# Optimization experiments

Hardware: AMD Instinct MI355X
Metric: run time of the kernel (lower is better)

## Reference

```python
import jax, jax.numpy as jnp
import numpy as np

N_EMBED = 16384
CODE_DIM = 32

def l2norm(t, eps=1e-12):
    return t / jnp.clip(jnp.linalg.norm(t, axis=-1, keepdims=True), eps)

def setup_inputs() -> dict:
    key = jax.random.key(0)
    k1, k2 = jax.random.split(key)
    z = jax.random.normal(k1, (8, 1024, CODE_DIM), dtype=jnp.float32)
    codebook = l2norm(jax.random.normal(k2, (N_EMBED, CODE_DIM), dtype=jnp.float32))
    return {"z": z, "codebook": codebook}

def reference(z, codebook):
    # z: [B, S, D]; codebook: [N, D]
    zn = l2norm(z)
    zf = zn.reshape(-1, zn.shape[-1])  # [B*S, D]
    d = (jnp.sum(zf * zf, axis=1, keepdims=True)
         + jnp.sum(codebook * codebook, axis=1)
         - 2.0 * jnp.einsum('bd,nd->bn', zf, codebook))  # [B*S, N]
    encoding_indices = jnp.argmin(d, axis=1)  # [B*S]
    z_q = codebook[encoding_indices]  # [B*S, D]
    return z_q, encoding_indices
```

## Files before the change

### kernel.cpp

```cpp
#include <hip/hip_runtime.h>
#include <math.h>

#define M_ROWS   8192
#define N_CODES  16384
#define D_DIM    32
#define NTHREADS 256

#define DELTA_MARGIN  2e-4f

#define NCHUNK       16
#define CHUNK_CODES  (N_CODES / NCHUNK)
#define SCAN_SLOTS   256

typedef short bf16x8 __attribute__((ext_vector_type(8)));
typedef float f32x4  __attribute__((ext_vector_type(4)));

__device__ inline unsigned short bf16_rne(float f) {
    unsigned u = __float_as_uint(f);
    unsigned r = u + 0x7FFFu + ((u >> 16) & 1u);
    return (unsigned short)(r >> 16);
}

__device__ inline void pack_pair(float f0, float f1, unsigned& hi, unsigned& lo) {
    unsigned short h0 = bf16_rne(f0), h1 = bf16_rne(f1);
    float r0 = f0 - __uint_as_float((unsigned)h0 << 16);
    float r1 = f1 - __uint_as_float((unsigned)h1 << 16);
    unsigned short l0 = bf16_rne(r0), l1 = bf16_rne(r1);
    hi = (unsigned)h0 | ((unsigned)h1 << 16);
    lo = (unsigned)l0 | ((unsigned)l1 << 16);
}

__global__ void vq_prep_pack(const float* __restrict__ z,
                             const float* __restrict__ codebook,
                             float* __restrict__ zn, float* __restrict__ zz,
                             float* __restrict__ cc,
                             unsigned* __restrict__ chi, unsigned* __restrict__ clo,
                             unsigned* __restrict__ zhi, unsigned* __restrict__ zlo,
                             int* __restrict__ todo_cnt) {
    int gid = blockIdx.x * NTHREADS + threadIdx.x;
    if (gid == 0) *todo_cnt = 0;
    if (blockIdx.x < 64) {
        const float4* r4 = reinterpret_cast<const float4*>(codebook + (size_t)gid * D_DIM);
        float4 v[8];
#pragma unroll
        for (int h = 0; h < 8; ++h) v[h] = r4[h];
        float s = 0.f;
#pragma unroll
        for (int h = 0; h < 8; ++h) {
            s = fmaf(v[h].x, v[h].x, s);
            s = fmaf(v[h].y, v[h].y, s);
            s = fmaf(v[h].z, v[h].z, s);
            s = fmaf(v[h].w, v[h].w, s);
        }
        cc[gid] = s;
#pragma unroll
        for (int h = 0; h < 8; ++h) {
            unsigned hi0, lo0, hi1, lo1;
            pack_pair(v[h].x, v[h].y, hi0, lo0);
            pack_pair(v[h].z, v[h].w, hi1, lo1);
            chi[gid * 16 + 2 * h]     = hi0;  clo[gid * 16 + 2 * h]     = lo0;
            chi[gid * 16 + 2 * h + 1] = hi1;  clo[gid * 16 + 2 * h + 1] = lo1;
        }
    } else {
        int r = gid - N_CODES;
        const float4* r4 = reinterpret_cast<const float4*>(z + (size_t)r * D_DIM);
        float4 v[8];
#pragma unroll
        for (int h = 0; h < 8; ++h) v[h] = r4[h];
        float s = 0.f;
#pragma unroll
        for (int h = 0; h < 8; ++h) {
            s = fmaf(v[h].x, v[h].x, s);
            s = fmaf(v[h].y, v[h].y, s);
            s = fmaf(v[h].z, v[h].z, s);
            s = fmaf(v[h].w, v[h].w, s);
        }
        float norm = sqrtf(s);
        norm = fmaxf(norm, 1e-12f);
        float zs = 0.f;
        float4* zn4 = reinterpret_cast<float4*>(zn + (size_t)r * D_DIM);
#pragma unroll
        for (int h = 0; h < 8; ++h) {
            float4 w;
            w.x = v[h].x / norm;
            w.y = v[h].y / norm;
            w.z = v[h].z / norm;
            w.w = v[h].w / norm;
            zn4[h] = w;
            zs = fmaf(w.x, w.x, zs);
            zs = fmaf(w.y, w.y, zs);
            zs = fmaf(w.z, w.z, zs);
            zs = fmaf(w.w, w.w, zs);
            v[h] = w;
        }
        zz[r] = zs;
#pragma unroll
        for (int h = 0; h < 8; ++h) {
            unsigned hi0, lo0, hi1, lo1;
            pack_pair(v[h].x, v[h].y, hi0, lo0);
            pack_pair(v[h].z, v[h].w, hi1, lo1);
            zhi[r * 16 + 2 * h]     = hi0;  zlo[r * 16 + 2 * h]     = lo0;
            zhi[r * 16 + 2 * h + 1] = hi1;  zlo[r * 16 + 2 * h + 1] = lo1;
        }
    }
}

template <int NS>
__global__ __launch_bounds__(NTHREADS, 4)
void vq_mfma(const unsigned short* __restrict__ zhi,
             const unsigned short* __restrict__ zlo,
             const unsigned short* __restrict__ chi,
             const unsigned short* __restrict__ clo,
             float* __restrict__ pmax1, float* __restrict__ pmax2,
             int* __restrict__ pidx) {
    constexpr int SLICE_CODES = N_CODES / NS;
    constexpr int NPAIR = SLICE_CODES / 32;

    const int tid  = threadIdx.x;
    const int wave = tid >> 6;
    const int lane = tid & 63;
    const int rb    = blockIdx.x & 63;
    const int slice = blockIdx.x >> 6;

    const int row_w = rb * 128 + wave * 32;
    const int l15 = lane & 15;
    const int kg  = lane >> 4;
    const int kc  = kg * 8;

    const bf16x8 a_hi0 = *reinterpret_cast<const bf16x8*>(zhi + (size_t)(row_w + l15) * 32 + kc);
    const bf16x8 a_lo0 = *reinterpret_cast<const bf16x8*>(zlo + (size_t)(row_w + l15) * 32 + kc);
    const bf16x8 a_hi1 = *reinterpret_cast<const bf16x8*>(zhi + (size_t)(row_w + 16 + l15) * 32 + kc);
    const bf16x8 a_lo1 = *reinterpret_cast<const bf16x8*>(zlo + (size_t)(row_w + 16 + l15) * 32 + kc);

    const f32x4 zero4 = {0.f, 0.f, 0.f, 0.f};

    float max1[8], max2[8];
    int   idx1[8];
#pragma unroll
    for (int q = 0; q < 8; ++q) { max1[q] = -3.4e38f; max2[q] = -3.4e38f; idx1[q] = 0x7FFFFFFF; }

    auto argup = [&](const f32x4& accA, const f32x4& accB, int code) {
#pragma unroll
        for (int e = 0; e < 4; ++e) {
            float s0 = accA[e];
            max2[e] = __builtin_amdgcn_fmed3f(s0, max1[e], max2[e]);
            bool gt0 = s0 > max1[e];
            max1[e] = gt0 ? s0 : max1[e];
            idx1[e] = gt0 ? code : idx1[e];

            float s1 = accB[e];
            max2[4 + e] = __builtin_amdgcn_fmed3f(s1, max1[4 + e], max2[4 + e]);
            bool gt1 = s1 > max1[4 + e];
            max1[4 + e] = gt1 ? s1 : max1[4 + e];
            idx1[4 + e] = gt1 ? code : idx1[4 + e];
        }
    };
    auto pair_compute = [&](const bf16x8& b0h, const bf16x8& b0l,
                            const bf16x8& b1h, const bf16x8& b1l, int code) {
        f32x4 a00 = __builtin_amdgcn_mfma_f32_16x16x32_bf16(a_lo0, b0h, zero4, 0, 0, 0);
        f32x4 a01 = __builtin_amdgcn_mfma_f32_16x16x32_bf16(a_lo1, b0h, zero4, 0, 0, 0);
        f32x4 a10 = __builtin_amdgcn_mfma_f32_16x16x32_bf16(a_lo0, b1h, zero4, 0, 0, 0);
        f32x4 a11 = __builtin_amdgcn_mfma_f32_16x16x32_bf16(a_lo1, b1h, zero4, 0, 0, 0);
        a00 = __builtin_amdgcn_mfma_f32_16x16x32_bf16(a_hi0, b0l, a00, 0, 0, 0);
        a01 = __builtin_amdgcn_mfma_f32_16x16x32_bf16(a_hi1, b0l, a01, 0, 0, 0);
        a10 = __builtin_amdgcn_mfma_f32_16x16x32_bf16(a_hi0, b1l, a10, 0, 0, 0);
        a11 = __builtin_amdgcn_mfma_f32_16x16x32_bf16(a_hi1, b1l, a11, 0, 0, 0);
        a00 = __builtin_amdgcn_mfma_f32_16x16x32_bf16(a_hi0, b0h, a00, 0, 0, 0);
        a01 = __builtin_amdgcn_mfma_f32_16x16x32_bf16(a_hi1, b0h, a01, 0, 0, 0);
        a10 = __builtin_amdgcn_mfma_f32_16x16x32_bf16(a_hi0, b1h, a10, 0, 0, 0);
        a11 = __builtin_amdgcn_mfma_f32_16x16x32_bf16(a_hi1, b1h, a11, 0, 0, 0);
        argup(a00, a01, code);
        argup(a10, a11, code + 16);
    };

    int code = slice * SLICE_CODES + l15;
    bf16x8 b0h = *reinterpret_cast<const bf16x8*>(chi + (size_t)code * 32 + kc);
    bf16x8 b0l = *reinterpret_cast<const bf16x8*>(clo + (size_t)code * 32 + kc);
    bf16x8 b1h = *reinterpret_cast<const bf16x8*>(chi + (size_t)(code + 16) * 32 + kc);
    bf16x8 b1l = *reinterpret_cast<const bf16x8*>(clo + (size_t)(code + 16) * 32 + kc);

    for (int p = 0; p < NPAIR - 1; ++p) {
        const int ncode = code + 32;
        const bf16x8 nb0h = *reinterpret_cast<const bf16x8*>(chi + (size_t)ncode * 32 + kc);
        const bf16x8 nb0l = *reinterpret_cast<const bf16x8*>(clo + (size_t)ncode * 32 + kc);
        const bf16x8 nb1h = *reinterpret_cast<const bf16x8*>(chi + (size_t)(ncode + 16) * 32 + kc);
        const bf16x8 nb1l = *reinterpret_cast<const bf16x8*>(clo + (size_t)(ncode + 16) * 32 + kc);

        pair_compute(b0h, b0l, b1h, b1l, code);

        b0h = nb0h; b0l = nb0l; b1h = nb1h; b1l = nb1l; code = ncode;
    }
    pair_compute(b0h, b0l, b1h, b1l, code);

#pragma unroll
    for (int q = 0; q < 8; ++q) {
        float m1 = max1[q], m2 = max2[q];
        int   i1 = idx1[q];
#pragma unroll
        for (int off = 1; off < 16; off <<= 1) {
            float o1 = __shfl_xor(m1, off);
            float o2 = __shfl_xor(m2, off);
            int   oi = __shfl_xor(i1, off);
            float nm2 = fmaxf(fminf(m1, o1), fmaxf(m2, o2));
            if (o1 > m1 || (o1 == m1 && oi < i1)) { m1 = o1; i1 = oi; }
            m2 = nm2;
        }
        max1[q] = m1; max2[q] = m2; idx1[q] = i1;
    }
    if (l15 == 0) {
#pragma unroll
        for (int q = 0; q < 8; ++q) {
            const int rt = q >> 2, e = q & 3;
            const int row = row_w + rt * 16 + kg * 4 + e;
            pmax1[slice * M_ROWS + row] = max1[q];
            pmax2[slice * M_ROWS + row] = max2[q];
            pidx [slice * M_ROWS + row] = idx1[q];
        }
    }
}

template <int NS>
__global__ void vq_merge(const float* __restrict__ codebook,
                         const float* __restrict__ pmax1,
                         const float* __restrict__ pmax2,
                         const int* __restrict__ pidx,
                         float* __restrict__ zq, float* __restrict__ idx_out,
                         int* __restrict__ todo_cnt, int* __restrict__ todo) {
    const int row = blockIdx.x * NTHREADS + threadIdx.x;
    float m1 = pmax1[row], m2 = pmax2[row];
    int   i1 = pidx[row];
#pragma unroll
    for (int s = 1; s < NS; ++s) {
        float o1 = pmax1[s * M_ROWS + row];
        float o2 = pmax2[s * M_ROWS + row];
        int   oi = pidx [s * M_ROWS + row];
        float nm2 = fmaxf(fminf(m1, o1), fmaxf(m2, o2));
        if (o1 > m1) { m1 = o1; i1 = oi; }
        m2 = nm2;
    }
    if (2.0f * (m1 - m2) > DELTA_MARGIN) {
        idx_out[row] = (float)i1;
        const float4* src = reinterpret_cast<const float4*>(codebook + (size_t)i1 * D_DIM);
        float4* dst = reinterpret_cast<float4*>(zq + (size_t)row * D_DIM);
#pragma unroll
        for (int k = 0; k < 8; ++k) dst[k] = src[k];
    } else {
        int p = atomicAdd(todo_cnt, 1);
        todo[p] = row;
    }
}

__global__ __launch_bounds__(NTHREADS)
void vq_cleanup_scan(const float* __restrict__ zn, const float* __restrict__ zz,
                     const float* __restrict__ codebook, const float* __restrict__ cc,
                     const int* __restrict__ todo_cnt, const int* __restrict__ todo,
                     float* __restrict__ cpmin, int* __restrict__ cpidx) {
    const int n = *todo_cnt;
    const int chunk = blockIdx.x & (NCHUNK - 1);
    const int slot  = blockIdx.x >> 4;
    const int tid   = threadIdx.x;
    const int cbase = chunk * CHUNK_CODES;

    __shared__ float sv[4];
    __shared__ int   si[4];

    for (int i = slot; i < n; i += SCAN_SLOTS) {
        const int row = todo[i];

        float zr[D_DIM];
#pragma unroll
        for (int d = 0; d < D_DIM; ++d) zr[d] = zn[(size_t)row * D_DIM + d];
        const float zzv = zz[row];

        float bm = 3.4e38f;
        int   bi = 0x7FFFFFFF;
#pragma unroll
        for (int k = 0; k < CHUNK_CODES / NTHREADS; ++k) {
            const int c = cbase + tid + (k << 8);
            const float4* cb = reinterpret_cast<const float4*>(codebook + (size_t)c * D_DIM);
            float dot = 0.f;
#pragma unroll
            for (int h = 0; h < 8; ++h) {
                float4 v = cb[h];
                dot = fmaf(zr[4 * h + 0], v.x, dot);
                dot = fmaf(zr[4 * h + 1], v.y, dot);
                dot = fmaf(zr[4 * h + 2], v.z, dot);
                dot = fmaf(zr[4 * h + 3], v.w, dot);
            }
            float t = zzv + cc[c];
            float dist = fmaf(-2.f, dot, t);
            if (dist < bm || (dist == bm && c < bi)) { bm = dist; bi = c; }
        }

#pragma unroll
        for (int off = 32; off >= 1; off >>= 1) {
            float ov = __shfl_xor(bm, off);
            int   oi = __shfl_xor(bi, off);
            if (ov < bm || (ov == bm && oi < bi)) { bm = ov; bi = oi; }
        }
        if ((tid & 63) == 0) { sv[tid >> 6] = bm; si[tid >> 6] = bi; }
        __syncthreads();
        if (tid == 0) {
            float v = sv[0]; int idx = si[0];
#pragma unroll
            for (int w = 1; w < 4; ++w) {
                if (sv[w] < v || (sv[w] == v && si[w] < idx)) { v = sv[w]; idx = si[w]; }
            }
            cpmin[chunk * M_ROWS + row] = v;
            cpidx[chunk * M_ROWS + row] = idx;
        }
        __syncthreads();
    }
}

__global__ __launch_bounds__(NTHREADS)
void vq_cleanup_final(const float* __restrict__ codebook,
                      const int* __restrict__ todo_cnt, const int* __restrict__ todo,
                      const float* __restrict__ cpmin, const int* __restrict__ cpidx,
                      float* __restrict__ zq, float* __restrict__ idx_out) {
    const int n = *todo_cnt;
    for (int i = blockIdx.x * NTHREADS + threadIdx.x; i < n; i += gridDim.x * NTHREADS) {
        const int row = todo[i];
        float bv = cpmin[row];
        int   bi = cpidx[row];
#pragma unroll
        for (int c = 1; c < NCHUNK; ++c) {
            float v = cpmin[c * M_ROWS + row];
            int   j = cpidx[c * M_ROWS + row];
            if (v < bv || (v == bv && j < bi)) { bv = v; bi = j; }
        }
        idx_out[row] = (float)bi;
        const float4* src = reinterpret_cast<const float4*>(codebook + (size_t)bi * D_DIM);
        float4* dst = reinterpret_cast<float4*>(zq + (size_t)row * D_DIM);
#pragma unroll
        for (int k = 0; k < 8; ++k) dst[k] = src[k];
    }
}

#define R_TILE   32
#define NSLICE_F 4
#define SLICE_CODES_F (N_CODES / NSLICE_F)
#define C_TILE   256
#define N_TILES_F (SLICE_CODES_F / C_TILE)
#define CB_PAD   36

__global__ void vq_prep_basic(const float* __restrict__ z,
                              const float* __restrict__ codebook,
                              float* __restrict__ zn,
                              float* __restrict__ zz,
                              float* __restrict__ cc) {
    int gid = blockIdx.x * NTHREADS + threadIdx.x;
    if (blockIdx.x < 64) {
        const float* row = codebook + (size_t)gid * D_DIM;
        float s = 0.f;
#pragma unroll
        for (int d = 0; d < D_DIM; ++d) s = fmaf(row[d], row[d], s);
        cc[gid] = s;
    } else {
        int r = gid - N_CODES;
        const float* row = z + (size_t)r * D_DIM;
        float s = 0.f;
#pragma unroll
        for (int d = 0; d < D_DIM; ++d) { float v = row[d]; s = fmaf(v, v, s); }
        float norm = sqrtf(s);
        norm = fmaxf(norm, 1e-12f);
        float zs = 0.f;
#pragma unroll
        for (int d = 0; d < D_DIM; ++d) {
            float v = row[d] / norm;
            zn[(size_t)r * D_DIM + d] = v;
            zs = fmaf(v, v, zs);
        }
        zz[r] = zs;
    }
}

__global__ __launch_bounds__(NTHREADS, 4)
void vq_main_basic(const float* __restrict__ zn, const float* __restrict__ zz,
                   const float* __restrict__ codebook, const float* __restrict__ cc,
                   float* __restrict__ pminv, int* __restrict__ pmini) {
    __shared__ float cb_lds[C_TILE * CB_PAD];
    __shared__ float zt[R_TILE * D_DIM];
    const int tid = threadIdx.x;
    const int rb = blockIdx.x & 255;
    const int slice = blockIdx.x >> 8;
    const int rg = tid >> 6;
    const int cg = tid & 63;
    const int row_base = rb * R_TILE;
    const int code_base = slice * SLICE_CODES_F;
    const int wrow = row_base + rg * 8;
    {
        float4 v = *reinterpret_cast<const float4*>(zn + (size_t)row_base * D_DIM + tid * 4);
        *reinterpret_cast<float4*>(&zt[tid * 4]) = v;
    }
    float zzr[8];
#pragma unroll
    for (int r = 0; r < 8; ++r) zzr[r] = zz[wrow + r];
    float minv[8]; int mini[8];
#pragma unroll
    for (int r = 0; r < 8; ++r) { minv[r] = 3.4e38f; mini[r] = 0; }
    for (int t = 0; t < N_TILES_F; ++t) {
        const int base = code_base + t * C_TILE;
        __syncthreads();
        {
            const float4* src = reinterpret_cast<const float4*>(codebook + (size_t)(base + tid) * D_DIM);
            float* dstf = &cb_lds[tid * CB_PAD];
#pragma unroll
            for (int k = 0; k < 8; ++k) *reinterpret_cast<float4*>(dstf + k * 4) = src[k];
        }
        __syncthreads();
        float acc[8][4];
#pragma unroll
        for (int r = 0; r < 8; ++r)
#pragma unroll
            for (int j = 0; j < 4; ++j) acc[r][j] = 0.f;
#pragma unroll
        for (int dc = 0; dc < 8; ++dc) {
            float4 cb4[4];
#pragma unroll
            for (int j = 0; j < 4; ++j)
                cb4[j] = *reinterpret_cast<const float4*>(&cb_lds[(cg + 64 * j) * CB_PAD + dc * 4]);
#pragma unroll
            for (int r = 0; r < 8; ++r) {
                const float4 zv = *reinterpret_cast<const float4*>(&zt[(rg * 8 + r) * D_DIM + dc * 4]);
#pragma unroll
                for (int j = 0; j < 4; ++j) {
                    float a = acc[r][j];
                    a = fmaf(zv.x, cb4[j].x, a);
                    a = fmaf(zv.y, cb4[j].y, a);
                    a = fmaf(zv.z, cb4[j].z, a);
                    a = fmaf(zv.w, cb4[j].w, a);
                    acc[r][j] = a;
                }
            }
        }
#pragma unroll
        for (int j = 0; j < 4; ++j) {
            const int code = base + cg + 64 * j;
            const float ccj = cc[code];
#pragma unroll
            for (int r = 0; r < 8; ++r) {
                float tsum = zzr[r] + ccj;
                float dist = fmaf(-2.f, acc[r][j], tsum);
                if (dist < minv[r]) { minv[r] = dist; mini[r] = code; }
            }
        }
    }
#pragma unroll
    for (int r = 0; r < 8; ++r) {
        float v = minv[r]; int i = mini[r];
#pragma unroll
        for (int off = 32; off >= 1; off >>= 1) {
            float ov = __shfl_xor(v, off);
            int   oi = __shfl_xor(i, off);
            if (ov < v || (ov == v && oi < i)) { v = ov; i = oi; }
        }
        minv[r] = v; mini[r] = i;
    }
    if (cg == 0) {
#pragma unroll
        for (int r = 0; r < 8; ++r) {
            pminv[slice * M_ROWS + wrow + r] = minv[r];
            pmini[slice * M_ROWS + wrow + r] = mini[r];
        }
    }
}

__global__ void vq_final_basic(const float* __restrict__ codebook,
                               const float* __restrict__ pminv,
                               const int* __restrict__ pmini,
                               float* __restrict__ zq, float* __restrict__ idx_out) {
    int row = blockIdx.x * NTHREADS + threadIdx.x;
    float bv = pminv[row];
    int   bi = pmini[row];
#pragma unroll
    for (int s = 1; s < NSLICE_F; ++s) {
        float v = pminv[s * M_ROWS + row];
        int   i = pmini[s * M_ROWS + row];
        if (v < bv || (v == bv && i < bi)) { bv = v; bi = i; }
    }
    idx_out[row] = (float)bi;
    const float4* src = reinterpret_cast<const float4*>(codebook + (size_t)bi * D_DIM);
    float4* dst = reinterpret_cast<float4*>(zq + (size_t)row * D_DIM);
#pragma unroll
    for (int k = 0; k < 8; ++k) dst[k] = src[k];
}

static size_t ws_needed(int nslice) {
    return 4ull * (N_CODES + M_ROWS + 3ull * (size_t)nslice * M_ROWS) +
           4ull * (4 + M_ROWS) +
           2ull * (2ull * N_CODES * D_DIM + 2ull * M_ROWS * D_DIM);
}

template <int NS>
static void launch_mfma_path(const float* z, const float* codebook,
                             float* zn, float* zq_out, float* idx_out,
                             void* d_ws, hipStream_t stream) {
    float* cc    = (float*)d_ws;
    float* zz    = cc + N_CODES;
    float* pmax1 = zz + M_ROWS;
    float* pmax2 = pmax1 + (size_t)NS * M_ROWS;
    int*   pidx  = (int*)(pmax2 + (size_t)NS * M_ROWS);
    int*   todo_cnt = pidx + (size_t)NS * M_ROWS;
    int*   todo  = todo_cnt + 4;
    unsigned* chi = (unsigned*)(todo + M_ROWS);
    unsigned* clo = chi + (size_t)N_CODES * D_DIM / 2;
    unsigned* zhi = clo + (size_t)N_CODES * D_DIM / 2;
    unsigned* zlo = zhi + (size_t)M_ROWS * D_DIM / 2;

    float* cpmin = pmax1;
    int*   cpidx = pidx;

    vq_prep_pack<<<96, NTHREADS, 0, stream>>>(z, codebook, zn, zz, cc,
                                              chi, clo, zhi, zlo, todo_cnt);
    vq_mfma<NS><<<64 * NS, NTHREADS, 0, stream>>>(
        (const unsigned short*)zhi, (const unsigned short*)zlo,
        (const unsigned short*)chi, (const unsigned short*)clo,
        pmax1, pmax2, pidx);
    vq_merge<NS><<<M_ROWS / NTHREADS, NTHREADS, 0, stream>>>(
        codebook, pmax1, pmax2, pidx, zq_out, idx_out, todo_cnt, todo);
    vq_cleanup_scan<<<SCAN_SLOTS * NCHUNK, NTHREADS, 0, stream>>>(
        zn, zz, codebook, cc, todo_cnt, todo, cpmin, cpidx);
    vq_cleanup_final<<<32, NTHREADS, 0, stream>>>(
        codebook, todo_cnt, todo, cpmin, cpidx, zq_out, idx_out);
}

extern "C" void kernel_launch(void* const* d_in, const int* in_sizes, int n_in,
                              void* d_out, int out_size, void* d_ws, size_t ws_size,
                              hipStream_t stream) {
    const float* z        = (const float*)d_in[0];
    const float* codebook = (const float*)d_in[1];

    float* out     = (float*)d_out;
    float* zq_out  = out;
    float* idx_out = out + (size_t)M_ROWS * D_DIM;
    float* zn      = zq_out;

    if (ws_size >= ws_needed(16)) {
        launch_mfma_path<16>(z, codebook, zn, zq_out, idx_out, d_ws, stream);
    } else {
        float* cc    = (float*)d_ws;
        float* zz    = cc + N_CODES;
        float* pminv = zz + M_ROWS;
        int*   pmini = (int*)(pminv + (size_t)NSLICE_F * M_ROWS);

        vq_prep_basic<<<96, NTHREADS, 0, stream>>>(z, codebook, zn, zz, cc);
        vq_main_basic<<<256 * NSLICE_F, NTHREADS, 0, stream>>>(zn, zz, codebook, cc,
                                                               pminv, pmini);
        vq_final_basic<<<M_ROWS / NTHREADS, NTHREADS, 0, stream>>>(codebook, pminv,
                                                                   pmini, zq_out, idx_out);
    }
}
```

Measured before the change: 73.82 us.

## Add lo*lo MFMA term, tighten margin, widen prep, use atomicMin cleanup

Adds the lo*lo split-bf16 product to the MFMA dot product, which makes it more accurate, and tightens the ambiguity margin so fewer rows go to the exact fp32 rescan. The prep kernel now uses four threads per row, and each thread packs a quarter of the row, which quadruples the grid. The cleanup scan replaces its shared-memory reduction and per-chunk partial arrays with packed 64-bit keys merged by atomicMin, which drops the barriers and the 16-way final merge. The cost is four extra MFMAs per pair in the main loop and redundant row loads in prep.

```diff
diff --git a/kernel.cpp b/kernel.cpp
--- a/kernel.cpp
+++ b/kernel.cpp
@@ -6,7 +6,7 @@
 #define D_DIM    32
 #define NTHREADS 256
 
-#define DELTA_MARGIN  2e-4f
+#define DELTA_MARGIN  8e-5f
 
 #define NCHUNK       16
 #define CHUNK_CODES  (N_CODES / NCHUNK)
@@ -30,6 +30,11 @@
     lo = (unsigned)l0 | ((unsigned)l1 << 16);
 }
 
+__device__ inline unsigned sortable_u32(float f) {
+    unsigned u = __float_as_uint(f);
+    return (u & 0x80000000u) ? ~u : (u | 0x80000000u);
+}
+
 __global__ void vq_prep_pack(const float* __restrict__ z,
                              const float* __restrict__ codebook,
                              float* __restrict__ zn, float* __restrict__ zz,
@@ -37,10 +42,13 @@
                              unsigned* __restrict__ chi, unsigned* __restrict__ clo,
                              unsigned* __restrict__ zhi, unsigned* __restrict__ zlo,
                              int* __restrict__ todo_cnt) {
-    int gid = blockIdx.x * NTHREADS + threadIdx.x;
+    int gid  = blockIdx.x * NTHREADS + threadIdx.x;
+    int row  = gid >> 2;
+    int part = gid & 3;
     if (gid == 0) *todo_cnt = 0;
-    if (blockIdx.x < 64) {
-        const float4* r4 = reinterpret_cast<const float4*>(codebook + (size_t)gid * D_DIM);
+
+    if (row < N_CODES) {
+        const float4* r4 = reinterpret_cast<const float4*>(codebook + (size_t)row * D_DIM);
         float4 v[8];
 #pragma unroll
         for (int h = 0; h < 8; ++h) v[h] = r4[h];
@@ -52,17 +60,18 @@
             s = fmaf(v[h].z, v[h].z, s);
             s = fmaf(v[h].w, v[h].w, s);
         }
-        cc[gid] = s;
-#pragma unroll
-        for (int h = 0; h < 8; ++h) {
+        if (part == 0) cc[row] = s;
+#pragma unroll
+        for (int k = 0; k < 2; ++k) {
+            int h = part * 2 + k;
             unsigned hi0, lo0, hi1, lo1;
             pack_pair(v[h].x, v[h].y, hi0, lo0);
             pack_pair(v[h].z, v[h].w, hi1, lo1);
-            chi[gid * 16 + 2 * h]     = hi0;  clo[gid * 16 + 2 * h]     = lo0;
-            chi[gid * 16 + 2 * h + 1] = hi1;  clo[gid * 16 + 2 * h + 1] = lo1;
+            chi[row * 16 + 2 * h]     = hi0;  clo[row * 16 + 2 * h]     = lo0;
+            chi[row * 16 + 2 * h + 1] = hi1;  clo[row * 16 + 2 * h + 1] = lo1;
         }
     } else {
-        int r = gid - N_CODES;
+        int r = row - N_CODES;
         const float4* r4 = reinterpret_cast<const float4*>(z + (size_t)r * D_DIM);
         float4 v[8];
 #pragma unroll
@@ -78,27 +87,27 @@
         float norm = sqrtf(s);
         norm = fmaxf(norm, 1e-12f);
         float zs = 0.f;
+        float4 w[8];
+#pragma unroll
+        for (int h = 0; h < 8; ++h) {
+            w[h].x = v[h].x / norm;
+            w[h].y = v[h].y / norm;
+            w[h].z = v[h].z / norm;
+            w[h].w = v[h].w / norm;
+            zs = fmaf(w[h].x, w[h].x, zs);
+            zs = fmaf(w[h].y, w[h].y, zs);
+            zs = fmaf(w[h].z, w[h].z, zs);
+            zs = fmaf(w[h].w, w[h].w, zs);
+        }
+        if (part == 0) zz[r] = zs;
         float4* zn4 = reinterpret_cast<float4*>(zn + (size_t)r * D_DIM);
 #pragma unroll
-        for (int h = 0; h < 8; ++h) {
-            float4 w;
-            w.x = v[h].x / norm;
-            w.y = v[h].y / norm;
-            w.z = v[h].z / norm;
-            w.w = v[h].w / norm;
-            zn4[h] = w;
-            zs = fmaf(w.x, w.x, zs);
-            zs = fmaf(w.y, w.y, zs);
-            zs = fmaf(w.z, w.z, zs);
-            zs = fmaf(w.w, w.w, zs);
-            v[h] = w;
-        }
-        zz[r] = zs;
-#pragma unroll
-        for (int h = 0; h < 8; ++h) {
+        for (int k = 0; k < 2; ++k) {
+            int h = part * 2 + k;
+            zn4[h] = w[h];
             unsigned hi0, lo0, hi1, lo1;
-            pack_pair(v[h].x, v[h].y, hi0, lo0);
-            pack_pair(v[h].z, v[h].w, hi1, lo1);
+            pack_pair(w[h].x, w[h].y, hi0, lo0);
+            pack_pair(w[h].z, w[h].w, hi1, lo1);
             zhi[r * 16 + 2 * h]     = hi0;  zlo[r * 16 + 2 * h]     = lo0;
             zhi[r * 16 + 2 * h + 1] = hi1;  zlo[r * 16 + 2 * h + 1] = lo1;
         }
@@ -157,10 +166,14 @@
     };
     auto pair_compute = [&](const bf16x8& b0h, const bf16x8& b0l,
                             const bf16x8& b1h, const bf16x8& b1l, int code) {
-        f32x4 a00 = __builtin_amdgcn_mfma_f32_16x16x32_bf16(a_lo0, b0h, zero4, 0, 0, 0);
-        f32x4 a01 = __builtin_amdgcn_mfma_f32_16x16x32_bf16(a_lo1, b0h, zero4, 0, 0, 0);
-        f32x4 a10 = __builtin_amdgcn_mfma_f32_16x16x32_bf16(a_lo0, b1h, zero4, 0, 0, 0);
-        f32x4 a11 = __builtin_amdgcn_mfma_f32_16x16x32_bf16(a_lo1, b1h, zero4, 0, 0, 0);
+        f32x4 a00 = __builtin_amdgcn_mfma_f32_16x16x32_bf16(a_lo0, b0l, zero4, 0, 0, 0);
+        f32x4 a01 = __builtin_amdgcn_mfma_f32_16x16x32_bf16(a_lo1, b0l, zero4, 0, 0, 0);
+        f32x4 a10 = __builtin_amdgcn_mfma_f32_16x16x32_bf16(a_lo0, b1l, zero4, 0, 0, 0);
+        f32x4 a11 = __builtin_amdgcn_mfma_f32_16x16x32_bf16(a_lo1, b1l, zero4, 0, 0, 0);
+        a00 = __builtin_amdgcn_mfma_f32_16x16x32_bf16(a_lo0, b0h, a00, 0, 0, 0);
+        a01 = __builtin_amdgcn_mfma_f32_16x16x32_bf16(a_lo1, b0h, a01, 0, 0, 0);
+        a10 = __builtin_amdgcn_mfma_f32_16x16x32_bf16(a_lo0, b1h, a10, 0, 0, 0);
+        a11 = __builtin_amdgcn_mfma_f32_16x16x32_bf16(a_lo1, b1h, a11, 0, 0, 0);
         a00 = __builtin_amdgcn_mfma_f32_16x16x32_bf16(a_hi0, b0l, a00, 0, 0, 0);
         a01 = __builtin_amdgcn_mfma_f32_16x16x32_bf16(a_hi1, b0l, a01, 0, 0, 0);
         a10 = __builtin_amdgcn_mfma_f32_16x16x32_bf16(a_hi0, b1l, a10, 0, 0, 0);
@@ -225,7 +238,8 @@
                          const float* __restrict__ pmax2,
                          const int* __restrict__ pidx,
                          float* __restrict__ zq, float* __restrict__ idx_out,
-                         int* __restrict__ todo_cnt, int* __restrict__ todo) {
+                         int* __restrict__ todo_cnt, int* __restrict__ todo,
+                         unsigned long long* __restrict__ rbest) {
     const int row = blockIdx.x * NTHREADS + threadIdx.x;
     float m1 = pmax1[row], m2 = pmax2[row];
     int   i1 = pidx[row];
@@ -245,6 +259,7 @@
 #pragma unroll
         for (int k = 0; k < 8; ++k) dst[k] = src[k];
     } else {
+        rbest[row] = 0xFFFFFFFFFFFFFFFFull;
         int p = atomicAdd(todo_cnt, 1);
         todo[p] = row;
     }
@@ -254,16 +269,13 @@
 void vq_cleanup_scan(const float* __restrict__ zn, const float* __restrict__ zz,
                      const float* __restrict__ codebook, const float* __restrict__ cc,
                      const int* __restrict__ todo_cnt, const int* __restrict__ todo,
-                     float* __restrict__ cpmin, int* __restrict__ cpidx) {
+                     unsigned long long* __restrict__ rbest) {
     const int n = *todo_cnt;
     const int chunk = blockIdx.x & (NCHUNK - 1);
     const int slot  = blockIdx.x >> 4;
     const int tid   = threadIdx.x;
     const int cbase = chunk * CHUNK_CODES;
 
-    __shared__ float sv[4];
-    __shared__ int   si[4];
-
     for (int i = slot; i < n; i += SCAN_SLOTS) {
         const int row = todo[i];
 
@@ -272,8 +284,7 @@
         for (int d = 0; d < D_DIM; ++d) zr[d] = zn[(size_t)row * D_DIM + d];
         const float zzv = zz[row];
 
-        float bm = 3.4e38f;
-        int   bi = 0x7FFFFFFF;
+        unsigned long long best = 0xFFFFFFFFFFFFFFFFull;
 #pragma unroll
         for (int k = 0; k < CHUNK_CODES / NTHREADS; ++k) {
             const int c = cbase + tid + (k << 8);
@@ -289,46 +300,31 @@
             }
             float t = zzv + cc[c];
             float dist = fmaf(-2.f, dot, t);
-            if (dist < bm || (dist == bm && c < bi)) { bm = dist; bi = c; }
+            unsigned long long key =
+                ((unsigned long long)sortable_u32(dist) << 32) | (unsigned)c;
+            best = (key < best) ? key : best;
         }
 
 #pragma unroll
         for (int off = 32; off >= 1; off >>= 1) {
-            float ov = __shfl_xor(bm, off);
-            int   oi = __shfl_xor(bi, off);
-            if (ov < bm || (ov == bm && oi < bi)) { bm = ov; bi = oi; }
-        }
-        if ((tid & 63) == 0) { sv[tid >> 6] = bm; si[tid >> 6] = bi; }
-        __syncthreads();
-        if (tid == 0) {
-            float v = sv[0]; int idx = si[0];
-#pragma unroll
-            for (int w = 1; w < 4; ++w) {
-                if (sv[w] < v || (sv[w] == v && si[w] < idx)) { v = sv[w]; idx = si[w]; }
-            }
-            cpmin[chunk * M_ROWS + row] = v;
-            cpidx[chunk * M_ROWS + row] = idx;
-        }
-        __syncthreads();
+            unsigned long long ob = __shfl_xor(best, off);
+            best = (ob < best) ? ob : best;
+        }
+        if ((tid & 63) == 0) {
+            atomicMin(&rbest[row], best);
+        }
     }
 }
 
 __global__ __launch_bounds__(NTHREADS)
 void vq_cleanup_final(const float* __restrict__ codebook,
                       const int* __restrict__ todo_cnt, const int* __restrict__ todo,
-                      const float* __restrict__ cpmin, const int* __restrict__ cpidx,
+                      const unsigned long long* __restrict__ rbest,
                       float* __restrict__ zq, float* __restrict__ idx_out) {
     const int n = *todo_cnt;
     for (int i = blockIdx.x * NTHREADS + threadIdx.x; i < n; i += gridDim.x * NTHREADS) {
         const int row = todo[i];
-        float bv = cpmin[row];
-        int   bi = cpidx[row];
-#pragma unroll
-        for (int c = 1; c < NCHUNK; ++c) {
-            float v = cpmin[c * M_ROWS + row];
-            int   j = cpidx[c * M_ROWS + row];
-            if (v < bv || (v == bv && j < bi)) { bv = v; bi = j; }
-        }
+        const int bi = (int)(unsigned)(rbest[row] & 0xFFFFFFFFull);
         idx_out[row] = (float)bi;
         const float4* src = reinterpret_cast<const float4*>(codebook + (size_t)bi * D_DIM);
         float4* dst = reinterpret_cast<float4*>(zq + (size_t)row * D_DIM);
@@ -489,7 +485,8 @@
 static size_t ws_needed(int nslice) {
     return 4ull * (N_CODES + M_ROWS + 3ull * (size_t)nslice * M_ROWS) +
            4ull * (4 + M_ROWS) +
-           2ull * (2ull * N_CODES * D_DIM + 2ull * M_ROWS * D_DIM);
+           8ull * M_ROWS +
+           2ull * (2ull * N_CODES * D_DIM + 2ull * M_ROWS * D_DIM) + 4096;
 }
 
 template <int NS>
@@ -503,26 +500,24 @@
     int*   pidx  = (int*)(pmax2 + (size_t)NS * M_ROWS);
     int*   todo_cnt = pidx + (size_t)NS * M_ROWS;
     int*   todo  = todo_cnt + 4;
-    unsigned* chi = (unsigned*)(todo + M_ROWS);
+    unsigned long long* rbest = (unsigned long long*)(todo + M_ROWS);
+    unsigned* chi = (unsigned*)(rbest + M_ROWS);
     unsigned* clo = chi + (size_t)N_CODES * D_DIM / 2;
     unsigned* zhi = clo + (size_t)N_CODES * D_DIM / 2;
     unsigned* zlo = zhi + (size_t)M_ROWS * D_DIM / 2;
 
-    float* cpmin = pmax1;
-    int*   cpidx = pidx;
-
-    vq_prep_pack<<<96, NTHREADS, 0, stream>>>(z, codebook, zn, zz, cc,
-                                              chi, clo, zhi, zlo, todo_cnt);
+    vq_prep_pack<<<384, NTHREADS, 0, stream>>>(z, codebook, zn, zz, cc,
+                                               chi, clo, zhi, zlo, todo_cnt);
     vq_mfma<NS><<<64 * NS, NTHREADS, 0, stream>>>(
         (const unsigned short*)zhi, (const unsigned short*)zlo,
         (const unsigned short*)chi, (const unsigned short*)clo,
         pmax1, pmax2, pidx);
     vq_merge<NS><<<M_ROWS / NTHREADS, NTHREADS, 0, stream>>>(
-        codebook, pmax1, pmax2, pidx, zq_out, idx_out, todo_cnt, todo);
+        codebook, pmax1, pmax2, pidx, zq_out, idx_out, todo_cnt, todo, rbest);
     vq_cleanup_scan<<<SCAN_SLOTS * NCHUNK, NTHREADS, 0, stream>>>(
-        zn, zz, codebook, cc, todo_cnt, todo, cpmin, cpidx);
+        zn, zz, codebook, cc, todo_cnt, todo, rbest);
     vq_cleanup_final<<<32, NTHREADS, 0, stream>>>(
-        codebook, todo_cnt, todo, cpmin, cpidx, zq_out, idx_out);
+        codebook, todo_cnt, todo, rbest, zq_out, idx_out);
 }
 
 extern "C" void kernel_launch(void* const* d_in, const int* in_sizes, int n_in,
```

Result: faster. 65.28 us, median of 2 (-11.6%).
